# Kernel tuning notes

Measured on AMD Instinct MI355X. Metric: run time of the kernel, lower is better.

## Reference

```python
import jax, jax.numpy as jnp
import numpy as np

# ---- config (matches init_kwargs) ----
DIM = 2048
N_HEADS = 16
Q_LORA = 1536
KV_LORA = 512
QK_NOPE = 128
QK_ROPE = 64
V_HEAD = 128
QK_HEAD = QK_NOPE + QK_ROPE  # 192
B, S = 2, 2048
EPS = 1e-6


def rmsnorm(x, w):
    return x * jax.lax.rsqrt(jnp.mean(x * x, axis=-1, keepdims=True) + EPS) * w


def apply_rotary_emb(x, freqs_cis):
    # x: (B, S, H, R) interleaved pairs; freqs_cis: (S, R//2, 2) = (cos, sin)
    xr = x.astype(jnp.float32).reshape(x.shape[:-1] + (-1, 2))
    cos = freqs_cis[None, :, None, :, 0]
    sin = freqs_cis[None, :, None, :, 1]
    out = jnp.stack(
        [xr[..., 0] * cos - xr[..., 1] * sin,
         xr[..., 1] * cos + xr[..., 0] * sin], axis=-1)
    return out.reshape(x.shape).astype(x.dtype)


def setup_inputs() -> dict:
    key = jax.random.key(0)
    ks = jax.random.split(key, 12)
    sc = lambda fan_in: 1.0 / np.sqrt(fan_in)

    x = jax.random.normal(ks[0], (B, S, DIM), jnp.float32)

    # RoPE table: (S, QK_ROPE//2, 2)
    inv_freq = 1.0 / (10000.0 ** (jnp.arange(0, QK_ROPE, 2, dtype=jnp.float32) / QK_ROPE))
    t = jnp.arange(S, dtype=jnp.float32)
    ang = jnp.einsum('s,r->sr', t, inv_freq)
    freqs_cis = jnp.stack([jnp.cos(ang), jnp.sin(ang)], axis=-1)

    # causal mask (S, T)
    mask = jnp.triu(jnp.full((S, S), -jnp.inf, dtype=jnp.float32), 1)

    params = {
        'wq_a_w': jax.random.normal(ks[1], (Q_LORA, DIM), jnp.float32) * sc(DIM),
        'wq_a_b': jnp.zeros((Q_LORA,), jnp.float32),
        'q_norm_w': jnp.ones((Q_LORA,), jnp.float32),
        'wq_b_w': jax.random.normal(ks[2], (N_HEADS * QK_HEAD, Q_LORA), jnp.float32) * sc(Q_LORA),
        'wq_b_b': jnp.zeros((N_HEADS * QK_HEAD,), jnp.float32),
        'wkv_a_w': jax.random.normal(ks[3], (KV_LORA + QK_ROPE, DIM), jnp.float32) * sc(DIM),
        'wkv_a_b': jnp.zeros((KV_LORA + QK_ROPE,), jnp.float32),
        'kv_norm_w': jnp.ones((KV_LORA,), jnp.float32),
        'wkv_b_w': jax.random.normal(ks[4], (N_HEADS * (QK_NOPE + V_HEAD), KV_LORA), jnp.float32) * sc(KV_LORA),
        'wo_w': jax.random.normal(ks[5], (DIM, N_HEADS * V_HEAD), jnp.float32) * sc(N_HEADS * V_HEAD),
        'wo_b': jnp.zeros((DIM,), jnp.float32),
    }
    return {'x': x, 'freqs_cis': freqs_cis, 'mask': mask, 'start_pos': 0, **params}


def reference(x, freqs_cis, mask, wq_a_w, wq_a_b, q_norm_w, wq_b_w, wq_b_b,
              wkv_a_w, wkv_a_b, kv_norm_w, wkv_b_w, wo_w, wo_b, start_pos):
    bsz, seqlen, _ = x.shape
    scale = QK_HEAD ** (-0.5)

    # q path (low-rank)
    q = rmsnorm(x @ wq_a_w.T + wq_a_b, q_norm_w) @ wq_b_w.T + wq_b_b
    q = q.reshape(bsz, seqlen, N_HEADS, QK_HEAD)
    q_nope, q_pe = q[..., :QK_NOPE], q[..., QK_NOPE:]
    q_pe = apply_rotary_emb(q_pe, freqs_cis)

    # kv path
    kv = x @ wkv_a_w.T + wkv_a_b
    kv, k_pe = kv[..., :KV_LORA], kv[..., KV_LORA:]
    k_pe = apply_rotary_emb(k_pe[:, :, None, :], freqs_cis)[:, :, 0, :]  # (B,T,R)

    # absorption: fold W_UK into q_nope
    wkv_b = wkv_b_w.reshape(N_HEADS, QK_NOPE + V_HEAD, KV_LORA)
    q_nope = jnp.einsum('bshd,hdc->bshc', q_nope, wkv_b[:, :QK_NOPE])
    kv_cache = rmsnorm(kv, kv_norm_w)  # (B,T,C)

    scores = (jnp.einsum('bshc,btc->bsht', q_nope, kv_cache)
              + jnp.einsum('bshr,btr->bsht', q_pe, k_pe)) * scale
    scores = scores + mask[:, None, :]
    attn = jax.nn.softmax(scores.astype(jnp.float32), axis=-1).astype(x.dtype)

    out = jnp.einsum('bsht,btc->bshc', attn, kv_cache)
    out = jnp.einsum('bshc,hdc->bshd', out, wkv_b[:, -V_HEAD:])
    out = out.reshape(bsz, seqlen, N_HEADS * V_HEAD) @ wo_w.T + wo_b
    return out
```

## Files before the change

### kernel.cpp

```cpp
#include <hip/hip_runtime.h>
#include <math.h>

#define B_    2
#define S_    2048
#define M_TOT 4096
#define DIM_  2048
#define NH_   16
#define QL_   1536
#define KVL_  512
#define QKN_  128
#define QKR_  64
#define VH_   128
#define QKH_  192
#define QSTR  3072
#define QP_STR 584

typedef short s16x8 __attribute__((ext_vector_type(8)));
typedef float f32x4 __attribute__((ext_vector_type(4)));
typedef unsigned short u16;
#define AS1 __attribute__((address_space(1)))
#define AS3 __attribute__((address_space(3)))

__device__ inline u16 f2bf(float f) {
    unsigned u = __float_as_uint(f);
    unsigned r = u + 0x7FFFu + ((u >> 16) & 1u);
    return (u16)(r >> 16);
}
__device__ inline float bf2f(u16 h) { return __uint_as_float(((unsigned)h) << 16); }

__device__ __forceinline__ void ld_lds16(const u16* g, u16* l) {
    __builtin_amdgcn_global_load_lds((const AS1 unsigned*)g, (AS3 unsigned*)l, 16, 0, 0);
}
#define BARW4 do { asm volatile("s_waitcnt vmcnt(4) lgkmcnt(0)" ::: "memory"); __builtin_amdgcn_s_barrier(); } while (0)
#define BARW2 do { asm volatile("s_waitcnt vmcnt(2) lgkmcnt(0)" ::: "memory"); __builtin_amdgcn_s_barrier(); } while (0)
#define BARW0 do { asm volatile("s_waitcnt vmcnt(0) lgkmcnt(0)" ::: "memory"); __builtin_amdgcn_s_barrier(); } while (0)
#define BARLG do { asm volatile("s_waitcnt lgkmcnt(0)" ::: "memory"); __builtin_amdgcn_s_barrier(); } while (0)

__global__ __launch_bounds__(256)
void gemm_bf16(const u16* __restrict__ A, const u16* __restrict__ Bm,
               const float* __restrict__ bias, void* __restrict__ Cv,
               int M, int N, int K, int ldA, int ldB, int ldC,
               long long sAz, long long sBz, long long sCz,
               float alpha, int outF32)
{
    __shared__ u16 As[128 * 32];
    __shared__ u16 Bs[128 * 32];
    const int tid = threadIdx.x;
    const int w = tid >> 6, l = tid & 63;
    const int m0 = blockIdx.y * 128, n0 = blockIdx.x * 128;
    const int z = blockIdx.z;
    const u16* Az = A + (size_t)z * sAz;
    const u16* Bz = Bm + (size_t)z * sBz;

    const int rin = l >> 2;
    const int cel = (l & 3) * 8;
    const int lane15 = l & 15, quad = l >> 4;
    const int wm = w & 1, wn = w >> 1;

    f32x4 acc[4][4] = {};

    for (int k0 = 0; k0 < K; k0 += 32) {
        __syncthreads();
        #pragma unroll
        for (int c = 0; c < 2; ++c) {
            const int chunk = w * 2 + c;
            const int rowA = m0 + chunk * 16 + rin;
            const u16* ga = Az + (size_t)rowA * ldA + k0 + cel;
            u16* la = &As[chunk * 512 + rin * 32 + cel];
            __builtin_amdgcn_global_load_lds((const AS1 unsigned*)ga, (AS3 unsigned*)la, 16, 0, 0);
            int rowB = n0 + chunk * 16 + rin;
            if (rowB > N - 1) rowB = N - 1;
            const u16* gb = Bz + (size_t)rowB * ldB + k0 + cel;
            u16* lb = &Bs[chunk * 512 + rin * 32 + cel];
            __builtin_amdgcn_global_load_lds((const AS1 unsigned*)gb, (AS3 unsigned*)lb, 16, 0, 0);
        }
        __syncthreads();
        s16x8 af[4], bf[4];
        #pragma unroll
        for (int i = 0; i < 4; ++i)
            af[i] = *(const s16x8*)&As[(wm * 64 + i * 16 + lane15) * 32 + quad * 8];
        #pragma unroll
        for (int i = 0; i < 4; ++i)
            bf[i] = *(const s16x8*)&Bs[(wn * 64 + i * 16 + lane15) * 32 + quad * 8];
        #pragma unroll
        for (int mi = 0; mi < 4; ++mi)
            #pragma unroll
            for (int ni = 0; ni < 4; ++ni)
                acc[mi][ni] = __builtin_amdgcn_mfma_f32_16x16x32_bf16(af[mi], bf[ni], acc[mi][ni], 0, 0, 0);
    }

    const int cmb = m0 + wm * 64, cnb = n0 + wn * 64;
    if (outF32) {
        float* C = (float*)Cv + (size_t)z * sCz;
        #pragma unroll
        for (int mi = 0; mi < 4; ++mi)
            #pragma unroll
            for (int ni = 0; ni < 4; ++ni) {
                const int nn = cnb + ni * 16 + lane15;
                if (nn < N) {
                    const float bv = bias ? bias[nn] : 0.f;
                    #pragma unroll
                    for (int r = 0; r < 4; ++r) {
                        const int mm = cmb + mi * 16 + quad * 4 + r;
                        C[(size_t)mm * ldC + nn] = acc[mi][ni][r] * alpha + bv;
                    }
                }
            }
    } else {
        u16* C = (u16*)Cv + (size_t)z * sCz;
        #pragma unroll
        for (int mi = 0; mi < 4; ++mi)
            #pragma unroll
            for (int ni = 0; ni < 4; ++ni) {
                const int nn = cnb + ni * 16 + lane15;
                if (nn < N) {
                    const float bv = bias ? bias[nn] : 0.f;
                    #pragma unroll
                    for (int r = 0; r < 4; ++r) {
                        const int mm = cmb + mi * 16 + quad * 4 + r;
                        C[(size_t)mm * ldC + nn] = f2bf(acc[mi][ni][r] * alpha + bv);
                    }
                }
            }
    }
}

__global__ __launch_bounds__(512)
void mla_flash(u16* __restrict__ Qp, const u16* __restrict__ Kcat,
               const u16* __restrict__ KVT)
{
    __shared__ u16 sQ[64 * QP_STR];
    __shared__ u16 sKV[4 * 8192];
    __shared__ u16 sP[64 * 136];
    __shared__ float sRm[64 * 4];
    __shared__ float sRs[64 * 4];
    __shared__ float sM[64], sL[64];

    const int tid = threadIdx.x;
    const int w = tid >> 6, l = tid & 63;
    const int lane15 = l & 15, quad = l >> 4;
    const int wq = w & 1;
    const int wk = w >> 1;

    const int flat = blockIdx.x;
    const int xcd  = flat & 7;
    const int slot = flat >> 3;
    const int b    = xcd >> 2;
    const int h    = (xcd & 3) * 4 + (slot & 3);
    const int qt   = 31 - (slot >> 2);
    const int qs   = qt * 64;

    u16* Qrow = Qp + ((size_t)h * M_TOT + b * S_ + qs) * 576;
    const float scale = 0.07216878364870323f;
    const u16* Kb = Kcat + (size_t)b * S_ * 576;
    const u16* Vb = KVT + (size_t)b * 512 * S_;

    const int seg8 = (tid & 3) * 8;
    const int sx8  = (((tid & 3) ^ ((tid >> 3) & 3)) * 8);
    const int qx8  = ((quad ^ ((lane15 >> 1) & 3)) * 8);
    const int ktiles = (qs + 64 + 127) >> 7;

    auto issueK = [&](int kt, int j, int buf) {
        const int key = tid >> 2;
        const u16* g = Kb + (size_t)(kt + key) * 576 + j * 64 + sx8;
        u16* d = &sKV[(buf << 13) + key * 32 + seg8];
        ld_lds16(g, d);
        ld_lds16(g + 32, d + 4096);
    };
    auto issueV = [&](int kt, int tc, int hf, int buf) {
        const int rl = tid >> 2;
        const u16* g = Vb + (size_t)(hf * 256 + rl) * S_ + kt + tc * 32 + sx8;
        u16* d = &sKV[(buf << 13) + rl * 32 + seg8];
        ld_lds16(g, d);
        ld_lds16(g + (size_t)128 * S_, d + 4096);
    };
    auto scoreC = [&](int j, int buf, f32x4 (&Sacc)[2][2]) {
        const u16* base = &sKV[buf << 13];
        __builtin_amdgcn_s_setprio(1);
        #pragma unroll
        for (int kk = 0; kk < 2; ++kk) {
            s16x8 af[2], bf[2];
            #pragma unroll
            for (int mi = 0; mi < 2; ++mi)
                af[mi] = *(const s16x8*)&sQ[(wq * 32 + mi * 16 + lane15) * QP_STR + j * 64 + kk * 32 + quad * 8];
            #pragma unroll
            for (int ni = 0; ni < 2; ++ni)
                bf[ni] = *(const s16x8*)&base[kk * 4096 + (wk * 32 + ni * 16 + lane15) * 32 + qx8];
            #pragma unroll
            for (int mi = 0; mi < 2; ++mi)
                #pragma unroll
                for (int ni = 0; ni < 2; ++ni)
                    Sacc[mi][ni] = __builtin_amdgcn_mfma_f32_16x16x32_bf16(af[mi], bf[ni], Sacc[mi][ni], 0, 0, 0);
        }
        __builtin_amdgcn_s_setprio(0);
    };

    issueK(0, 0, 0);
    issueK(0, 1, 1);
    issueK(0, 2, 2);
    {
        const int r = tid >> 3, c0 = (tid & 7) * 8;
        #pragma unroll
        for (int jj = 0; jj < 9; ++jj) {
            const int c = c0 + jj * 64;
            *(s16x8*)&sQ[r * QP_STR + c] = *(const s16x8*)&Qrow[(size_t)r * 576 + c];
        }
    }
    if (tid < 64) { sM[tid] = -1e30f; sL[tid] = 0.f; }
    BARW4;

    f32x4 Oacc[2][8] = {};

    for (int t = 0; t < ktiles; ++t) {
        const int kt = t << 7;
        const int tb = t & 3;
        const bool hn = (t + 1 < ktiles);
        f32x4 Sacc[2][2] = {};

        #pragma unroll
        for (int s = 0; s < 6; ++s) {
            issueK(kt, s + 3, (tb + s + 3) & 3);
            scoreC(s, (tb + s) & 3, Sacc);
            BARW4;
        }
        scoreC(6, (tb + 6) & 3, Sacc);
        BARW2;
        issueV(kt, 0, 0, (tb + 9) & 3);
        scoreC(7, (tb + 7) & 3, Sacc);
        BARW2;
        issueV(kt, 0, 1, (tb + 10) & 3);
        scoreC(8, (tb + 8) & 3, Sacc);
        #pragma unroll
        for (int mi = 0; mi < 2; ++mi)
            #pragma unroll
            for (int r = 0; r < 4; ++r) {
                const int rowl = wq * 32 + mi * 16 + quad * 4 + r;
                const int rowg = qs + rowl;
                float mx = -1e30f;
                #pragma unroll
                for (int ni = 0; ni < 2; ++ni) {
                    const int colg = kt + wk * 32 + ni * 16 + lane15;
                    float v = Sacc[mi][ni][r] * scale;
                    v = (colg <= rowg) ? v : -1e30f;
                    Sacc[mi][ni][r] = v;
                    mx = fmaxf(mx, v);
                }
                #pragma unroll
                for (int sh = 1; sh < 16; sh <<= 1) mx = fmaxf(mx, __shfl_xor(mx, sh));
                if (lane15 == 0) sRm[rowl * 4 + wk] = mx;
            }
        BARW2;

        issueV(kt, 1, 0, (tb + 11) & 3);
        float mn_[2][4], al_[2][4];
        #pragma unroll
        for (int mi = 0; mi < 2; ++mi)
            #pragma unroll
            for (int r = 0; r < 4; ++r) {
                const int rowl = wq * 32 + mi * 16 + quad * 4 + r;
                const f32x4 pm = *(const f32x4*)&sRm[rowl * 4];
                const float m_old = sM[rowl];
                const float mn = fmaxf(fmaxf(fmaxf(pm[0], pm[1]), fmaxf(pm[2], pm[3])), m_old);
                const float al = __expf(m_old - mn);
                mn_[mi][r] = mn; al_[mi][r] = al;
                float sum = 0.f;
                #pragma unroll
                for (int ni = 0; ni < 2; ++ni) {
                    const float p = __expf(Sacc[mi][ni][r] - mn);
                    sP[rowl * 136 + wk * 32 + ni * 16 + lane15] = f2bf(p);
                    sum += p;
                }
                #pragma unroll
                for (int ci = 0; ci < 8; ++ci) Oacc[mi][ci][r] *= al;
                #pragma unroll
                for (int sh = 1; sh < 16; sh <<= 1) sum += __shfl_xor(sum, sh);
                if (lane15 == 0) sRs[rowl * 4 + wk] = sum;
            }
        BARLG;

        if (wk == 0 && lane15 == 0) {
            #pragma unroll
            for (int mi = 0; mi < 2; ++mi)
                #pragma unroll
                for (int r = 0; r < 4; ++r) {
                    const int rowl = wq * 32 + mi * 16 + quad * 4 + r;
                    const f32x4 ps = *(const f32x4*)&sRs[rowl * 4];
                    sL[rowl] = sL[rowl] * al_[mi][r] + (ps[0] + ps[1] + ps[2] + ps[3]);
                    sM[rowl] = mn_[mi][r];
                }
        }

        #pragma unroll
        for (int k = 0; k < 8; ++k) {
            const int cis = 12 + k;
            if (cis <= 16)      issueV(kt, (cis - 9) >> 1, (cis - 9) & 1, (tb + cis) & 3);
            else if (hn)        issueK(kt + 128, cis - 17, (tb + 1 + (cis - 17)) & 3);
            {
                const int tc = k >> 1, hf = k & 1;
                const u16* base = &sKV[(((tb + 9 + k) & 3)) << 13];
                s16x8 pf[2], vf[4];
                #pragma unroll
                for (int mi = 0; mi < 2; ++mi)
                    pf[mi] = *(const s16x8*)&sP[(wq * 32 + mi * 16 + lane15) * 136 + tc * 32 + quad * 8];
                #pragma unroll
                for (int ci = 0; ci < 4; ++ci) {
                    const int rl = wk * 64 + ci * 16 + lane15;
                    vf[ci] = *(const s16x8*)&base[rl * 32 + qx8];
                }
                __builtin_amdgcn_s_setprio(1);
                #pragma unroll
                for (int mi = 0; mi < 2; ++mi)
                    #pragma unroll
                    for (int ci = 0; ci < 4; ++ci)
                        Oacc[mi][hf * 4 + ci] = __builtin_amdgcn_mfma_f32_16x16x32_bf16(pf[mi], vf[ci], Oacc[mi][hf * 4 + ci], 0, 0, 0);
                __builtin_amdgcn_s_setprio(0);
            }
            if (k < 5 || hn) { BARW4; }
            else if (k == 5) { BARW2; }
            else if (k == 6) { BARW0; }
        }
    }

    #pragma unroll
    for (int mi = 0; mi < 2; ++mi)
        #pragma unroll
        for (int r = 0; r < 4; ++r) {
            const int rowl = wq * 32 + mi * 16 + quad * 4 + r;
            const float inv = 1.f / sL[rowl];
            #pragma unroll
            for (int hf = 0; hf < 2; ++hf)
                #pragma unroll
                for (int ci = 0; ci < 4; ++ci)
                    Qrow[(size_t)rowl * 576 + hf * 256 + wk * 64 + ci * 16 + lane15] =
                        f2bf(Oacc[mi][hf * 4 + ci][r] * inv);
        }
}

__global__ __launch_bounds__(256)
void cast_f32_bf16(const float* __restrict__ src, u16* __restrict__ dst, int n)
{
    for (int i = blockIdx.x * 256 + threadIdx.x; i < n; i += gridDim.x * 256)
        dst[i] = f2bf(src[i]);
}

__global__ __launch_bounds__(256)
void prep_wbnT(const float* __restrict__ wkvb, u16* __restrict__ dst)
{
    int i = blockIdx.x * 256 + threadIdx.x;
    int h = i >> 16, rem = i & 65535, c = rem >> 7, d = rem & 127;
    dst[i] = f2bf(wkvb[(size_t)(h * 256 + d) * 512 + c]);
}

__global__ __launch_bounds__(256)
void prep_wbv(const float* __restrict__ wkvb, u16* __restrict__ dst)
{
    int i = blockIdx.x * 256 + threadIdx.x;
    int h = i >> 16, rem = i & 65535;
    dst[i] = f2bf(wkvb[(size_t)h * 131072 + 65536 + rem]);
}

__global__ __launch_bounds__(256)
void rmsnorm_bf16(u16* __restrict__ X, const float* __restrict__ w, int D)
{
    const int m = blockIdx.x;
    u16* x = X + (size_t)m * D;
    float ss = 0.f;
    for (int k = threadIdx.x; k < D; k += 256) { float v = bf2f(x[k]); ss += v * v; }
    __shared__ float red[256];
    red[threadIdx.x] = ss; __syncthreads();
    for (int s = 128; s > 0; s >>= 1) {
        if (threadIdx.x < s) red[threadIdx.x] += red[threadIdx.x + s];
        __syncthreads();
    }
    const float sc = rsqrtf(red[0] / (float)D + 1e-6f);
    for (int k = threadIdx.x; k < D; k += 256) x[k] = f2bf(bf2f(x[k]) * sc * w[k]);
}

__global__ __launch_bounds__(256)
void rope_q(const u16* __restrict__ q, const float* __restrict__ freqs, u16* __restrict__ Qp)
{
    const int idx = blockIdx.x * 256 + threadIdx.x;
    const int i = idx & 31, h = (idx >> 5) & 15, m = idx >> 9;
    const int s = m & (S_ - 1);
    const float c = freqs[(s * 32 + i) * 2], sn = freqs[(s * 32 + i) * 2 + 1];
    const u16* src = q + (size_t)m * QSTR + h * QKH_ + QKN_ + 2 * i;
    const float x0 = bf2f(src[0]), x1 = bf2f(src[1]);
    u16* dst = Qp + ((size_t)h * M_TOT + m) * 576 + 512 + 2 * i;
    dst[0] = f2bf(x0 * c - x1 * sn);
    dst[1] = f2bf(x1 * c + x0 * sn);
}

__global__ __launch_bounds__(256)
void kv_norm_rope(const u16* __restrict__ kva, const float* __restrict__ w,
                  const float* __restrict__ freqs, u16* __restrict__ Kcat)
{
    const int m = blockIdx.x, s = m & (S_ - 1);
    const u16* x = kva + (size_t)m * 576;
    float ss = 0.f;
    for (int k = threadIdx.x; k < 512; k += 256) { float v = bf2f(x[k]); ss += v * v; }
    __shared__ float red[256];
    red[threadIdx.x] = ss; __syncthreads();
    for (int st = 128; st > 0; st >>= 1) {
        if (threadIdx.x < st) red[threadIdx.x] += red[threadIdx.x + st];
        __syncthreads();
    }
    const float sc = rsqrtf(red[0] / 512.f + 1e-6f);
    for (int k = threadIdx.x; k < 512; k += 256)
        Kcat[(size_t)m * 576 + k] = f2bf(bf2f(x[k]) * sc * w[k]);
    if (threadIdx.x < 32) {
        const int i = threadIdx.x;
        const float c = freqs[(s * 32 + i) * 2], sn = freqs[(s * 32 + i) * 2 + 1];
        const float x0 = bf2f(x[512 + 2 * i]), x1 = bf2f(x[512 + 2 * i + 1]);
        Kcat[(size_t)m * 576 + 512 + 2 * i]     = f2bf(x0 * c - x1 * sn);
        Kcat[(size_t)m * 576 + 512 + 2 * i + 1] = f2bf(x1 * c + x0 * sn);
    }
}

__global__ __launch_bounds__(256)
void transpose_kv(const u16* __restrict__ Kcat, u16* __restrict__ KVT)
{
    __shared__ u16 t[64][65];
    const int s0 = blockIdx.x * 64, c0 = blockIdx.y * 64, b = blockIdx.z;
    #pragma unroll
    for (int i = 0; i < 16; ++i) {
        int id = i * 256 + threadIdx.x, r = id >> 6, c = id & 63;
        t[r][c] = Kcat[(size_t)(b * S_ + s0 + r) * 576 + c0 + c];
    }
    __syncthreads();
    #pragma unroll
    for (int i = 0; i < 16; ++i) {
        int id = i * 256 + threadIdx.x, r = id >> 6, c = id & 63;
        KVT[(size_t)(b * 512 + c0 + r) * S_ + s0 + c] = t[c][r];
    }
}

extern "C" void kernel_launch(void* const* d_in, const int* in_sizes, int n_in,
                              void* d_out, int out_size, void* d_ws, size_t ws_size,
                              hipStream_t stream)
{
    (void)in_sizes; (void)n_in; (void)out_size; (void)ws_size;
    const float* x         = (const float*)d_in[0];
    const float* freqs     = (const float*)d_in[1];
    const float* wq_a_w    = (const float*)d_in[4];
    const float* wq_a_b    = (const float*)d_in[5];
    const float* q_norm_w  = (const float*)d_in[6];
    const float* wq_b_w    = (const float*)d_in[7];
    const float* wq_b_b    = (const float*)d_in[8];
    const float* wkv_a_w   = (const float*)d_in[9];
    const float* wkv_a_b   = (const float*)d_in[10];
    const float* kv_norm_w = (const float*)d_in[11];
    const float* wkv_b_w   = (const float*)d_in[12];
    const float* wo_w      = (const float*)d_in[13];
    const float* wo_b      = (const float*)d_in[14];
    float* out = (float*)d_out;

    char* W = (char*)d_ws;
    u16* x_bf  = (u16*)(W + 0);
    u16* wqa   = (u16*)(W + 16777216);
    u16* wqb   = (u16*)(W + 23068672);
    u16* wkva  = (u16*)(W + 32505856);
    u16* wobf  = (u16*)(W + 34865152);
    u16* wbnT  = (u16*)(W + 43253760);
    u16* wbv   = (u16*)(W + 45350912);
    u16* q_a   = (u16*)(W + 47448064);
    u16* q     = (u16*)(W + 60030976);
    u16* kv_a  = (u16*)(W + 85196800);
    u16* Kcat  = (u16*)(W + 89915392);
    u16* KVT   = (u16*)(W + 94633984);
    u16* Qp    = (u16*)(W + 98828288);
    u16* outh  = (u16*)(W + 174325760);

    const dim3 blk(256);

    cast_f32_bf16<<<2048, blk, 0, stream>>>(x, x_bf, M_TOT * DIM_);
    cast_f32_bf16<<<2048, blk, 0, stream>>>(wq_a_w, wqa, QL_ * DIM_);
    cast_f32_bf16<<<2048, blk, 0, stream>>>(wq_b_w, wqb, QSTR * QL_);
    cast_f32_bf16<<<2048, blk, 0, stream>>>(wkv_a_w, wkva, 576 * DIM_);
    cast_f32_bf16<<<2048, blk, 0, stream>>>(wo_w, wobf, DIM_ * DIM_);
    prep_wbnT<<<4096, blk, 0, stream>>>(wkv_b_w, wbnT);
    prep_wbv<<<4096, blk, 0, stream>>>(wkv_b_w, wbv);

    gemm_bf16<<<dim3(12, 32, 1), blk, 0, stream>>>(x_bf, wqa, wq_a_b, q_a,
        M_TOT, QL_, DIM_, DIM_, DIM_, QL_, 0, 0, 0, 1.f, 0);
    rmsnorm_bf16<<<M_TOT, blk, 0, stream>>>(q_a, q_norm_w, QL_);
    gemm_bf16<<<dim3(24, 32, 1), blk, 0, stream>>>(q_a, wqb, wq_b_b, q,
        M_TOT, QSTR, QL_, QL_, QL_, QSTR, 0, 0, 0, 1.f, 0);
    rope_q<<<(M_TOT * NH_ * 32) / 256, blk, 0, stream>>>(q, freqs, Qp);

    gemm_bf16<<<dim3(5, 32, 1), blk, 0, stream>>>(x_bf, wkva, wkv_a_b, kv_a,
        M_TOT, 576, DIM_, DIM_, DIM_, 576, 0, 0, 0, 1.f, 0);
    kv_norm_rope<<<M_TOT, blk, 0, stream>>>(kv_a, kv_norm_w, freqs, Kcat);
    transpose_kv<<<dim3(32, 8, 2), blk, 0, stream>>>(Kcat, KVT);

    gemm_bf16<<<dim3(4, 32, 16), blk, 0, stream>>>(q, wbnT, nullptr, Qp,
        M_TOT, 512, 128, QSTR, 128, 576, QKH_, 65536, (long long)M_TOT * 576, 1.f, 0);

    mla_flash<<<dim3(1024, 1, 1), dim3(512), 0, stream>>>(Qp, Kcat, KVT);

    gemm_bf16<<<dim3(1, 32, 16), blk, 0, stream>>>(Qp, wbv, nullptr, outh,
        M_TOT, VH_, 512, 576, 512, DIM_, (long long)M_TOT * 576, 65536, VH_, 1.f, 0);

    gemm_bf16<<<dim3(16, 32, 1), blk, 0, stream>>>(outh, wobf, wo_b, out,
        M_TOT, DIM_, DIM_, DIM_, DIM_, DIM_, 0, 0, 0, 1.f, 1);
}
```

Measured before the change: 924.5 us.

## Keep Q fragments in registers and restructure K/V LDS ring to three larger stages

Q tile fragments are now loaded straight from global memory into registers (36 s16x8 per lane) and the sQ shared buffer is removed. That LDS space goes to a 3-stage ring of 32KB slots, so each pipeline step stages a 96-column K chunk or a 512-row V chunk per 32-key column. Score and PV loops run 6 and 4 steps per tile instead of 9 and 8, with fewer barriers, and each wave now owns a contiguous 128-column output slice. The cost is much higher register pressure, which can lower occupancy or cause spills, plus more complex vmcnt accounting across the ring.

```diff
diff --git a/kernel.cpp b/kernel.cpp
--- a/kernel.cpp
+++ b/kernel.cpp
@@ -13,7 +13,6 @@
 #define VH_   128
 #define QKH_  192
 #define QSTR  3072
-#define QP_STR 584
 
 typedef short s16x8 __attribute__((ext_vector_type(8)));
 typedef float f32x4 __attribute__((ext_vector_type(4)));
@@ -31,8 +30,8 @@
 __device__ __forceinline__ void ld_lds16(const u16* g, u16* l) {
     __builtin_amdgcn_global_load_lds((const AS1 unsigned*)g, (AS3 unsigned*)l, 16, 0, 0);
 }
+#define BARW3 do { asm volatile("s_waitcnt vmcnt(3) lgkmcnt(0)" ::: "memory"); __builtin_amdgcn_s_barrier(); } while (0)
 #define BARW4 do { asm volatile("s_waitcnt vmcnt(4) lgkmcnt(0)" ::: "memory"); __builtin_amdgcn_s_barrier(); } while (0)
-#define BARW2 do { asm volatile("s_waitcnt vmcnt(2) lgkmcnt(0)" ::: "memory"); __builtin_amdgcn_s_barrier(); } while (0)
 #define BARW0 do { asm volatile("s_waitcnt vmcnt(0) lgkmcnt(0)" ::: "memory"); __builtin_amdgcn_s_barrier(); } while (0)
 #define BARLG do { asm volatile("s_waitcnt lgkmcnt(0)" ::: "memory"); __builtin_amdgcn_s_barrier(); } while (0)
 
@@ -129,8 +128,7 @@
 void mla_flash(u16* __restrict__ Qp, const u16* __restrict__ Kcat,
                const u16* __restrict__ KVT)
 {
-    __shared__ u16 sQ[64 * QP_STR];
-    __shared__ u16 sKV[4 * 8192];
+    __shared__ u16 sRing[3 * 16384];
     __shared__ u16 sP[64 * 136];
     __shared__ float sRm[64 * 4];
     __shared__ float sRs[64 * 4];
@@ -160,76 +158,68 @@
     const int qx8  = ((quad ^ ((lane15 >> 1) & 3)) * 8);
     const int ktiles = (qs + 64 + 127) >> 7;
 
-    auto issueK = [&](int kt, int j, int buf) {
+    auto issueK = [&](int kt, int j, int so) {
         const int key = tid >> 2;
-        const u16* g = Kb + (size_t)(kt + key) * 576 + j * 64 + sx8;
-        u16* d = &sKV[(buf << 13) + key * 32 + seg8];
+        const u16* g = Kb + (size_t)(kt + key) * 576 + j * 96 + sx8;
+        u16* d = &sRing[so + key * 32 + seg8];
         ld_lds16(g, d);
         ld_lds16(g + 32, d + 4096);
+        ld_lds16(g + 64, d + 8192);
     };
-    auto issueV = [&](int kt, int tc, int hf, int buf) {
+    auto issueV = [&](int kt, int tc, int so) {
         const int rl = tid >> 2;
-        const u16* g = Vb + (size_t)(hf * 256 + rl) * S_ + kt + tc * 32 + sx8;
-        u16* d = &sKV[(buf << 13) + rl * 32 + seg8];
+        const u16* g = Vb + (size_t)rl * S_ + kt + tc * 32 + sx8;
+        u16* d = &sRing[so + rl * 32 + seg8];
         ld_lds16(g, d);
         ld_lds16(g + (size_t)128 * S_, d + 4096);
+        ld_lds16(g + (size_t)256 * S_, d + 8192);
+        ld_lds16(g + (size_t)384 * S_, d + 12288);
     };
-    auto scoreC = [&](int j, int buf, f32x4 (&Sacc)[2][2]) {
-        const u16* base = &sKV[buf << 13];
-        __builtin_amdgcn_s_setprio(1);
-        #pragma unroll
-        for (int kk = 0; kk < 2; ++kk) {
-            s16x8 af[2], bf[2];
-            #pragma unroll
-            for (int mi = 0; mi < 2; ++mi)
-                af[mi] = *(const s16x8*)&sQ[(wq * 32 + mi * 16 + lane15) * QP_STR + j * 64 + kk * 32 + quad * 8];
-            #pragma unroll
-            for (int ni = 0; ni < 2; ++ni)
-                bf[ni] = *(const s16x8*)&base[kk * 4096 + (wk * 32 + ni * 16 + lane15) * 32 + qx8];
-            #pragma unroll
-            for (int mi = 0; mi < 2; ++mi)
-                #pragma unroll
-                for (int ni = 0; ni < 2; ++ni)
-                    Sacc[mi][ni] = __builtin_amdgcn_mfma_f32_16x16x32_bf16(af[mi], bf[ni], Sacc[mi][ni], 0, 0, 0);
-        }
-        __builtin_amdgcn_s_setprio(0);
-    };
-
+
+    s16x8 afq[2][18];
+    #pragma unroll
+    for (int mi = 0; mi < 2; ++mi) {
+        const u16* qsrc = Qrow + (size_t)(wq * 32 + mi * 16 + lane15) * 576 + quad * 8;
+        #pragma unroll
+        for (int c = 0; c < 18; ++c)
+            afq[mi][c] = *(const s16x8*)&qsrc[c * 32];
+    }
     issueK(0, 0, 0);
-    issueK(0, 1, 1);
-    issueK(0, 2, 2);
-    {
-        const int r = tid >> 3, c0 = (tid & 7) * 8;
-        #pragma unroll
-        for (int jj = 0; jj < 9; ++jj) {
-            const int c = c0 + jj * 64;
-            *(s16x8*)&sQ[r * QP_STR + c] = *(const s16x8*)&Qrow[(size_t)r * 576 + c];
-        }
-    }
+    issueK(0, 1, 16384);
     if (tid < 64) { sM[tid] = -1e30f; sL[tid] = 0.f; }
-    BARW4;
+    BARW3;
 
     f32x4 Oacc[2][8] = {};
 
     for (int t = 0; t < ktiles; ++t) {
         const int kt = t << 7;
-        const int tb = t & 3;
+        const int tb = t % 3;
         const bool hn = (t + 1 < ktiles);
         f32x4 Sacc[2][2] = {};
 
         #pragma unroll
-        for (int s = 0; s < 6; ++s) {
-            issueK(kt, s + 3, (tb + s + 3) & 3);
-            scoreC(s, (tb + s) & 3, Sacc);
-            BARW4;
+        for (int p = 0; p < 6; ++p) {
+            const int soI = ((tb + p + 2) % 3) * 16384;
+            if (p < 4) issueK(kt, p + 2, soI);
+            else       issueV(kt, p - 4, soI);
+            const u16* base = &sRing[((tb + p) % 3) * 16384];
+            __builtin_amdgcn_s_setprio(1);
+            #pragma unroll
+            for (int kk = 0; kk < 3; ++kk) {
+                s16x8 bf[2];
+                #pragma unroll
+                for (int ni = 0; ni < 2; ++ni)
+                    bf[ni] = *(const s16x8*)&base[kk * 4096 + (wk * 32 + ni * 16 + lane15) * 32 + qx8];
+                #pragma unroll
+                for (int mi = 0; mi < 2; ++mi)
+                    #pragma unroll
+                    for (int ni = 0; ni < 2; ++ni)
+                        Sacc[mi][ni] = __builtin_amdgcn_mfma_f32_16x16x32_bf16(afq[mi][p * 3 + kk], bf[ni], Sacc[mi][ni], 0, 0, 0);
+            }
+            __builtin_amdgcn_s_setprio(0);
+            if (p < 4) { BARW3; } else { BARW4; }
         }
-        scoreC(6, (tb + 6) & 3, Sacc);
-        BARW2;
-        issueV(kt, 0, 0, (tb + 9) & 3);
-        scoreC(7, (tb + 7) & 3, Sacc);
-        BARW2;
-        issueV(kt, 0, 1, (tb + 10) & 3);
-        scoreC(8, (tb + 8) & 3, Sacc);
+
         #pragma unroll
         for (int mi = 0; mi < 2; ++mi)
             #pragma unroll
@@ -249,9 +239,8 @@
                 for (int sh = 1; sh < 16; sh <<= 1) mx = fmaxf(mx, __shfl_xor(mx, sh));
                 if (lane15 == 0) sRm[rowl * 4 + wk] = mx;
             }
-        BARW2;
-
-        issueV(kt, 1, 0, (tb + 11) & 3);
+        BARLG;
+
         float mn_[2][4], al_[2][4];
         #pragma unroll
         for (int mi = 0; mi < 2; ++mi)
@@ -291,33 +280,49 @@
         }
 
         #pragma unroll
-        for (int k = 0; k < 8; ++k) {
-            const int cis = 12 + k;
-            if (cis <= 16)      issueV(kt, (cis - 9) >> 1, (cis - 9) & 1, (tb + cis) & 3);
-            else if (hn)        issueK(kt + 128, cis - 17, (tb + 1 + (cis - 17)) & 3);
+        for (int tc = 0; tc < 4; ++tc) {
+            const int p = 6 + tc;
+            const int soI = ((tb + p + 2) % 3) * 16384;
+            if (tc < 2)       issueV(kt, tc + 2, soI);
+            else if (hn)      issueK(kt + 128, tc - 2, soI);
+            const u16* base = &sRing[((tb + p) % 3) * 16384];
+            s16x8 pf[2];
+            #pragma unroll
+            for (int mi = 0; mi < 2; ++mi)
+                pf[mi] = *(const s16x8*)&sP[(wq * 32 + mi * 16 + lane15) * 136 + tc * 32 + quad * 8];
             {
-                const int tc = k >> 1, hf = k & 1;
-                const u16* base = &sKV[(((tb + 9 + k) & 3)) << 13];
-                s16x8 pf[2], vf[4];
-                #pragma unroll
-                for (int mi = 0; mi < 2; ++mi)
-                    pf[mi] = *(const s16x8*)&sP[(wq * 32 + mi * 16 + lane15) * 136 + tc * 32 + quad * 8];
+                s16x8 vf[4];
                 #pragma unroll
                 for (int ci = 0; ci < 4; ++ci) {
-                    const int rl = wk * 64 + ci * 16 + lane15;
-                    vf[ci] = *(const s16x8*)&base[rl * 32 + qx8];
+                    const int rl = wk * 128 + ci * 16 + lane15;
+                    vf[ci] = *(const s16x8*)&base[(rl >> 7) * 4096 + (rl & 127) * 32 + qx8];
                 }
                 __builtin_amdgcn_s_setprio(1);
                 #pragma unroll
                 for (int mi = 0; mi < 2; ++mi)
                     #pragma unroll
                     for (int ci = 0; ci < 4; ++ci)
-                        Oacc[mi][hf * 4 + ci] = __builtin_amdgcn_mfma_f32_16x16x32_bf16(pf[mi], vf[ci], Oacc[mi][hf * 4 + ci], 0, 0, 0);
+                        Oacc[mi][ci] = __builtin_amdgcn_mfma_f32_16x16x32_bf16(pf[mi], vf[ci], Oacc[mi][ci], 0, 0, 0);
                 __builtin_amdgcn_s_setprio(0);
             }
-            if (k < 5 || hn) { BARW4; }
-            else if (k == 5) { BARW2; }
-            else if (k == 6) { BARW0; }
+            {
+                s16x8 vf[4];
+                #pragma unroll
+                for (int ci = 0; ci < 4; ++ci) {
+                    const int rl = wk * 128 + (ci + 4) * 16 + lane15;
+                    vf[ci] = *(const s16x8*)&base[(rl >> 7) * 4096 + (rl & 127) * 32 + qx8];
+                }
+                __builtin_amdgcn_s_setprio(1);
+                #pragma unroll
+                for (int mi = 0; mi < 2; ++mi)
+                    #pragma unroll
+                    for (int ci = 0; ci < 4; ++ci)
+                        Oacc[mi][ci + 4] = __builtin_amdgcn_mfma_f32_16x16x32_bf16(pf[mi], vf[ci], Oacc[mi][ci + 4], 0, 0, 0);
+                __builtin_amdgcn_s_setprio(0);
+            }
+            if (tc < 2)      { BARW4; }
+            else if (tc == 2){ if (hn) { BARW3; } else { BARW0; } }
+            else             { if (hn) { BARW3; } else { BARLG; } }
         }
     }
 
@@ -328,11 +333,9 @@
             const int rowl = wq * 32 + mi * 16 + quad * 4 + r;
             const float inv = 1.f / sL[rowl];
             #pragma unroll
-            for (int hf = 0; hf < 2; ++hf)
-                #pragma unroll
-                for (int ci = 0; ci < 4; ++ci)
-                    Qrow[(size_t)rowl * 576 + hf * 256 + wk * 64 + ci * 16 + lane15] =
-                        f2bf(Oacc[mi][hf * 4 + ci][r] * inv);
+            for (int ci = 0; ci < 8; ++ci)
+                Qrow[(size_t)rowl * 576 + wk * 128 + ci * 16 + lane15] =
+                    f2bf(Oacc[mi][ci][r] * inv);
         }
 }
 
```

New measurement: 1.130 ms. 22.3% more time.
